# Optimization experiments

Hardware: AMD Instinct MI355X
Metric: run time of the kernel (lower is better)

The kernel has to match this reference:

```python
import jax, jax.numpy as jnp
import numpy as np

B, T, Z, S, H = 32, 128, 100, 6, 64
F1, F2 = 512, 128


def setup_inputs() -> dict:
    key = jax.random.key(0)
    ks = jax.random.split(key, 11)
    g = lambda k, shape, sc: (jax.random.normal(k, shape, dtype=jnp.float32) * sc)
    return {
        "x": jax.random.normal(ks[0], (B, T, Z, S), dtype=jnp.float32),
        "W_ih": g(ks[1], (3 * H, S), 0.125),   # GRU input weights [r|z|n]
        "W_hh": g(ks[2], (3 * H, H), 0.125),   # GRU hidden weights [r|z|n]
        "b_ih": g(ks[3], (3 * H,), 0.125),
        "b_hh": g(ks[4], (3 * H,), 0.125),
        "w1": g(ks[5], (F1, H), 0.1),
        "b1": g(ks[6], (F1,), 0.1),
        "w2": g(ks[7], (F2, F1), 0.04),
        "b2": g(ks[8], (F2,), 0.04),
        "w3": g(ks[9], (1, F2), 0.09),
        "b3": g(ks[10], (1,), 0.09),
    }


def reference(x, W_ih, W_hh, b_ih, b_hh, w1, b1, w2, b2, w3, b3):
    b, t, z, s = x.shape
    h_dim = W_hh.shape[1]
    # Fuse the per-zone python loop into the batch dim, zone-major so the
    # final reshape matches torch.stack(a).view(-1, t, nzones).
    xm = jnp.transpose(x, (2, 0, 1, 3)).reshape(z * b, t, s)  # (ZB, T, S)
    # Precompute input projections for all timesteps (one big GEMM).
    gi_all = jnp.einsum('nts,gs->ntg', xm, W_ih) + b_ih        # (ZB, T, 3H)

    def step(h, gi):
        gh = h @ W_hh.T + b_hh
        r = jax.nn.sigmoid(gi[:, :h_dim] + gh[:, :h_dim])
        zg = jax.nn.sigmoid(gi[:, h_dim:2 * h_dim] + gh[:, h_dim:2 * h_dim])
        n = jnp.tanh(gi[:, 2 * h_dim:] + r * gh[:, 2 * h_dim:])
        h_new = (1.0 - zg) * n + zg * h
        return h_new, h_new

    h0 = jnp.zeros((z * b, h_dim), x.dtype)
    _, sx = jax.lax.scan(step, h0, jnp.swapaxes(gi_all, 0, 1))  # (T, ZB, H)
    sx = jnp.swapaxes(sx, 0, 1)                                  # (ZB, T, H)

    a1 = jax.nn.relu(sx @ w1.T + b1)
    a2 = jax.nn.relu(a1 @ w2.T + b2)
    a3 = a2 @ w3.T + b3                                          # (ZB, T, 1)
    return a3.reshape(-1, t, z)                                  # (B, T, Z)
```

## Files before the change

### kernel.cpp

```cpp
#include <hip/hip_runtime.h>
#include <stdint.h>

#define Tdim 128
#define Zdim 100
#define Sdim 6
#define Hdim 64
#define ZB   3200
#define F1   512
#define F2   128
#define Mrows (ZB * Tdim)

typedef _Float16 f16x8 __attribute__((ext_vector_type(8)));
typedef _Float16 f16x4 __attribute__((ext_vector_type(4)));
typedef float f32x4 __attribute__((ext_vector_type(4)));
typedef uint32_t u32x4 __attribute__((ext_vector_type(4)));

__device__ __forceinline__ float sigmoidf_fast(float x) {
  return 1.f / (1.f + __expf(-x));
}
__device__ __forceinline__ float tanhf_fast(float x) {
  return 1.f - 2.f / (__expf(2.f * x) + 1.f);
}

__global__ __launch_bounds__(256) void prep_kernel(
    const float* __restrict__ W_ih, const float* __restrict__ W_hh,
    const float* __restrict__ w1, const float* __restrict__ w2,
    _Float16* __restrict__ Wf, _Float16* __restrict__ w1p,
    _Float16* __restrict__ w2p) {
  int i = blockIdx.x * 256 + threadIdx.x;
  if (i < 192 * 96) {
    int g = i / 96, k = i - g * 96;
    float v = (k < 64) ? W_hh[g * 64 + k] : ((k < 70) ? W_ih[g * 6 + (k - 64)] : 0.f);
    Wf[i] = (_Float16)v;
  }
  int j = i - 192 * 96;
  if (j >= 0 && j < 32768) {
    int kt = j >> 11, ntl = (j >> 10) & 1, kf = (j >> 9) & 1;
    int lane = (j >> 3) & 63, e = j & 7;
    int q = lane >> 4, c = lane & 15;
    int row = kt * 32 + ntl * 16 + c;
    int h = kf * 32 + q * 8 + e;
    w1p[j] = (_Float16)w1[row * 64 + h];
  }
  int l = j - 32768;
  if (l >= 0 && l < 65536) {
    int kt = l >> 12, nt = (l >> 9) & 7;
    int lane = (l >> 3) & 63, e = l & 7;
    int q = lane >> 4, c = lane & 15;
    int row = nt * 16 + c;
    int k = kt * 32 + q * 8 + e;
    w2p[l] = (_Float16)w2[row * 512 + k];
  }
}

__global__ __launch_bounds__(256, 1) void gru_kernel(
    const float* __restrict__ x, const _Float16* __restrict__ Wf,
    const float* __restrict__ b_ih, const float* __restrict__ b_hh,
    _Float16* __restrict__ sx) {
  __shared__ __align__(16) _Float16 hist[32][16][72];
  __shared__ __align__(16) _Float16 xs[Tdim][16][8];
  const int tid = threadIdx.x;
  const int lane = tid & 63;
  const int w = tid >> 6;
  const int c = lane & 15;
  const int q = lane >> 4;

  for (int i = 0; i < 8; i++) {
    int idx = i * 256 + tid;
    int t = idx >> 4, row = idx & 15;
    int nr = blockIdx.x * 16 + row;
    const float* p = x + (size_t)(nr & 31) * (Tdim * Zdim * Sdim)
                       + (size_t)t * (Zdim * Sdim) + (size_t)(nr >> 5) * Sdim;
    f16x8 v;
    v[0] = (_Float16)p[0]; v[1] = (_Float16)p[1]; v[2] = (_Float16)p[2];
    v[3] = (_Float16)p[3]; v[4] = (_Float16)p[4]; v[5] = (_Float16)p[5];
    v[6] = (_Float16)0.f;  v[7] = (_Float16)0.f;
    *(f16x8*)&xs[t][row][0] = v;
  }

  const int gr0 = w * 16;
  const int gz0 = 64 + w * 16;
  const int gn0 = 128 + w * 16;

  f16x8 Ar[3], Az[3], Anh[2], Ani;
#pragma unroll
  for (int kf = 0; kf < 3; kf++) {
    Ar[kf] = *(const f16x8*)(Wf + (size_t)(gr0 + c) * 96 + kf * 32 + q * 8);
    Az[kf] = *(const f16x8*)(Wf + (size_t)(gz0 + c) * 96 + kf * 32 + q * 8);
  }
  Anh[0] = *(const f16x8*)(Wf + (size_t)(gn0 + c) * 96 + q * 8);
  Anh[1] = *(const f16x8*)(Wf + (size_t)(gn0 + c) * 96 + 32 + q * 8);
  Ani    = *(const f16x8*)(Wf + (size_t)(gn0 + c) * 96 + 64 + q * 8);

  f32x4 Cr, Cz, Cnh, Cni;
  {
    f32x4 bir = *(const f32x4*)(b_ih + gr0 + q * 4);
    f32x4 bhr = *(const f32x4*)(b_hh + gr0 + q * 4);
    f32x4 biz = *(const f32x4*)(b_ih + gz0 + q * 4);
    f32x4 bhz = *(const f32x4*)(b_hh + gz0 + q * 4);
#pragma unroll
    for (int r = 0; r < 4; r++) { Cr[r] = bir[r] + bhr[r]; Cz[r] = biz[r] + bhz[r]; }
    Cnh = *(const f32x4*)(b_hh + gn0 + q * 4);
    Cni = *(const f32x4*)(b_ih + gn0 + q * 4);
  }

  __syncthreads();

  f16x8 Bh0 = {0, 0, 0, 0, 0, 0, 0, 0};
  f16x8 Bh1 = {0, 0, 0, 0, 0, 0, 0, 0};
  f32x4 hprev = {0.f, 0.f, 0.f, 0.f};
  const f32x4 zero4 = {0.f, 0.f, 0.f, 0.f};

  f32x4 Dr_s, Dz_s, Dni_s;
  {
    f16x8 xv8 = *(const f16x8*)&xs[0][c][0];
    f16x8 Bx;
#pragma unroll
    for (int j = 0; j < 8; j++) Bx[j] = (q == 0) ? xv8[j] : (_Float16)0.f;
    Dni_s = __builtin_amdgcn_mfma_f32_16x16x32_f16(Ani, Bx, Cni, 0, 0, 0);
    Dr_s  = __builtin_amdgcn_mfma_f32_16x16x32_f16(Ar[2], Bx, Cr, 0, 0, 0);
    Dz_s  = __builtin_amdgcn_mfma_f32_16x16x32_f16(Az[2], Bx, Cz, 0, 0, 0);
  }

#pragma unroll 1
  for (int tch = 0; tch < 4; tch++) {
#pragma unroll 1
    for (int tc = 0; tc < 32; tc++) {
      const int t = tch * 32 + tc;
      f32x4 Dnh0 = __builtin_amdgcn_mfma_f32_16x16x32_f16(Anh[0], Bh0, Cnh, 0, 0, 0);
      f32x4 Dr0  = __builtin_amdgcn_mfma_f32_16x16x32_f16(Ar[0], Bh0, Dr_s, 0, 0, 0);
      f32x4 Dz0  = __builtin_amdgcn_mfma_f32_16x16x32_f16(Az[0], Bh0, Dz_s, 0, 0, 0);
      f32x4 Dnh1 = __builtin_amdgcn_mfma_f32_16x16x32_f16(Anh[1], Bh1, zero4, 0, 0, 0);
      f32x4 Dr1  = __builtin_amdgcn_mfma_f32_16x16x32_f16(Ar[1], Bh1, zero4, 0, 0, 0);
      f32x4 Dz1  = __builtin_amdgcn_mfma_f32_16x16x32_f16(Az[1], Bh1, zero4, 0, 0, 0);

      f16x4 pk;
#pragma unroll
      for (int r = 0; r < 4; r++) {
        float rr = sigmoidf_fast(Dr0[r] + Dr1[r]);
        float zg = sigmoidf_fast(Dz0[r] + Dz1[r]);
        float nn = tanhf_fast(Dni_s[r] + rr * (Dnh0[r] + Dnh1[r]));
        float hnew = nn + zg * (hprev[r] - nn);
        hprev[r] = hnew;
        pk[r] = (_Float16)hnew;
      }
      *(f16x4*)&hist[tc][c][w * 16 + q * 4] = pk;

      if (t + 1 < Tdim) {
        f16x8 xv8 = *(const f16x8*)&xs[t + 1][c][0];
        f16x8 Bx;
#pragma unroll
        for (int j = 0; j < 8; j++) Bx[j] = (q == 0) ? xv8[j] : (_Float16)0.f;
        Dni_s = __builtin_amdgcn_mfma_f32_16x16x32_f16(Ani, Bx, Cni, 0, 0, 0);
        Dr_s  = __builtin_amdgcn_mfma_f32_16x16x32_f16(Ar[2], Bx, Cr, 0, 0, 0);
        Dz_s  = __builtin_amdgcn_mfma_f32_16x16x32_f16(Az[2], Bx, Cz, 0, 0, 0);
      }
      __syncthreads();
      Bh0 = *(const f16x8*)&hist[tc][c][q * 8];
      Bh1 = *(const f16x8*)&hist[tc][c][32 + q * 8];
    }
    {
      const int t0 = tch * 32;
#pragma unroll
      for (int rr2 = 0; rr2 < 4; rr2++) {
        const int row = w * 4 + rr2;
        const int nrow = blockIdx.x * 16 + row;
        _Float16* dst = sx + (size_t)nrow * Tdim * Hdim + (size_t)t0 * Hdim;
#pragma unroll
        for (int it = 0; it < 4; it++) {
          int idx = it * 64 + lane;
          int tcc = idx >> 3, hd8 = idx & 7;
          f16x8 vv = *(const f16x8*)&hist[tcc][row][hd8 * 8];
          *(f16x8*)(dst + tcc * 64 + hd8 * 8) = vv;
        }
      }
      __syncthreads();
    }
  }
}

__global__ __launch_bounds__(256, 2) void mlp_kernel(
    const _Float16* __restrict__ sx, const _Float16* __restrict__ w1p,
    const _Float16* __restrict__ w2p, const float* __restrict__ b1,
    const float* __restrict__ b2, const float* __restrict__ w3,
    const float* __restrict__ b3, float* __restrict__ out) {
  __shared__ __align__(16) _Float16 rep[4][4][512];
  const int tid = threadIdx.x;
  const int lane = tid & 63;
  const int wave = tid >> 6;
  const int c = lane & 15;
  const int q = lane >> 4;
  const size_t m0 = ((size_t)blockIdx.x * 4 + wave) * 64;

  f16x8 Bs[4][2];
#pragma unroll
  for (int g = 0; g < 4; g++)
#pragma unroll
    for (int kk = 0; kk < 2; kk++)
      Bs[g][kk] = *(const f16x8*)(sx + (m0 + g * 16 + c) * Hdim + kk * 32 + q * 8);

  f32x4 acc2[4][8];
#pragma unroll
  for (int g = 0; g < 4; g++)
#pragma unroll
    for (int nt = 0; nt < 8; nt++) acc2[g][nt] = (f32x4){0.f, 0.f, 0.f, 0.f};

#pragma unroll 2
  for (int kt = 0; kt < 16; kt++) {
    const _Float16* w1g = w1p + (size_t)kt * 2048 + lane * 8;
    const _Float16* w2g = w2p + (size_t)kt * 4096 + lane * 8;
    f16x8 A10 = *(const f16x8*)(w1g);
    f16x8 A11 = *(const f16x8*)(w1g + 512);
    f16x8 A12 = *(const f16x8*)(w1g + 1024);
    f16x8 A13 = *(const f16x8*)(w1g + 1536);

#pragma unroll
    for (int ntl = 0; ntl < 2; ntl++) {
      const int f1b = kt * 32 + ntl * 16;
      f16x8 A0 = ntl ? A12 : A10;
      f16x8 A1 = ntl ? A13 : A11;
      f32x4 bb = *(const f32x4*)(b1 + f1b + q * 4);
      const int roff = ((2 * ntl + (q >> 1)) * 16 + c) * 8 + (q & 1) * 4;
#pragma unroll
      for (int g = 0; g < 4; g++) {
        f32x4 cc = __builtin_amdgcn_mfma_f32_16x16x32_f16(A0, Bs[g][0], bb, 0, 0, 0);
        cc = __builtin_amdgcn_mfma_f32_16x16x32_f16(A1, Bs[g][1], cc, 0, 0, 0);
        f16x4 pk;
#pragma unroll
        for (int r = 0; r < 4; r++)
          pk[r] = (_Float16)(cc[r] > 0.f ? cc[r] : 0.f);
        *(f16x4*)&rep[wave][g][roff] = pk;
      }
    }
    f16x8 W2[8];
#pragma unroll
    for (int nt = 0; nt < 8; nt++)
      W2[nt] = *(const f16x8*)(w2g + nt * 512);
    f16x8 Ba[4];
#pragma unroll
    for (int g = 0; g < 4; g++)
      Ba[g] = *(const f16x8*)&rep[wave][g][lane * 8];
#pragma unroll
    for (int nt = 0; nt < 8; nt++) {
#pragma unroll
      for (int g = 0; g < 4; g++)
        acc2[g][nt] = __builtin_amdgcn_mfma_f32_16x16x32_f16(W2[nt], Ba[g], acc2[g][nt], 0, 0, 0);
    }
  }

  float part[4] = {0.f, 0.f, 0.f, 0.f};
#pragma unroll
  for (int nt = 0; nt < 8; nt++) {
    f32x4 bb = *(const f32x4*)(b2 + nt * 16 + q * 4);
    f32x4 ww = *(const f32x4*)(w3 + nt * 16 + q * 4);
#pragma unroll
    for (int g = 0; g < 4; g++) {
#pragma unroll
      for (int r = 0; r < 4; r++) {
        float v = acc2[g][nt][r] + bb[r];
        v = v > 0.f ? v : 0.f;
        part[g] = fmaf(v, ww[r], part[g]);
      }
    }
  }
#pragma unroll
  for (int g = 0; g < 4; g++) {
    part[g] += __shfl_xor(part[g], 16, 64);
    part[g] += __shfl_xor(part[g], 32, 64);
  }
  float pv = (q == 0) ? part[0] : (q == 1) ? part[1] : (q == 2) ? part[2] : part[3];
  out[m0 + q * 16 + c] = pv + b3[0];
}

extern "C" void kernel_launch(void* const* d_in, const int* in_sizes, int n_in,
                              void* d_out, int out_size, void* d_ws, size_t ws_size,
                              hipStream_t stream) {
  const float* x    = (const float*)d_in[0];
  const float* W_ih = (const float*)d_in[1];
  const float* W_hh = (const float*)d_in[2];
  const float* b_ih = (const float*)d_in[3];
  const float* b_hh = (const float*)d_in[4];
  const float* w1   = (const float*)d_in[5];
  const float* b1   = (const float*)d_in[6];
  const float* w2   = (const float*)d_in[7];
  const float* b2   = (const float*)d_in[8];
  const float* w3   = (const float*)d_in[9];
  const float* b3   = (const float*)d_in[10];
  float* out = (float*)d_out;

  char* ws = (char*)d_ws;
  _Float16* sxf = (_Float16*)ws;
  _Float16* Wf  = (_Float16*)(ws + 52428800);
  _Float16* w1p = (_Float16*)(ws + 52428800 + 36864);
  _Float16* w2p = (_Float16*)(ws + 52428800 + 36864 + 65536);

  hipLaunchKernelGGL(prep_kernel, dim3(456), dim3(256), 0, stream,
                     W_ih, W_hh, w1, w2, Wf, w1p, w2p);
  hipLaunchKernelGGL(gru_kernel, dim3(ZB / 16), dim3(256), 0, stream,
                     x, Wf, b_ih, b_hh, sxf);
  hipLaunchKernelGGL(mlp_kernel, dim3(Mrows / 256), dim3(256), 0, stream,
                     sxf, w1p, w2p, b1, b2, w3, b3, out);
}
```

Baseline: 257.9 us.

## Fuse GRU recurrence with MLP head, overlapping MLP on previous chunk

Merges the GRU and MLP kernels into one kernel. The MLP for the previous 16-timestep chunk runs interleaved with the serial GRU steps of the current chunk, using a double-buffered shared-memory history. This removes the 50 MB fp16 hidden-state round trip through global memory and uses idle MFMA/VALU slots in the latency-bound recurrence. The cost is that only 200 blocks do all the MLP work with one block per CU, and register pressure rises, which risks spills and a longer serial critical path.

```diff
diff --git a/kernel.cpp b/kernel.cpp
--- a/kernel.cpp
+++ b/kernel.cpp
@@ -8,12 +8,10 @@
 #define ZB   3200
 #define F1   512
 #define F2   128
-#define Mrows (ZB * Tdim)
 
 typedef _Float16 f16x8 __attribute__((ext_vector_type(8)));
 typedef _Float16 f16x4 __attribute__((ext_vector_type(4)));
 typedef float f32x4 __attribute__((ext_vector_type(4)));
-typedef uint32_t u32x4 __attribute__((ext_vector_type(4)));
 
 __device__ __forceinline__ float sigmoidf_fast(float x) {
   return 1.f / (1.f + __expf(-x));
@@ -53,12 +51,16 @@
   }
 }
 
-__global__ __launch_bounds__(256, 1) void gru_kernel(
+__global__ __launch_bounds__(256, 1) void fused_kernel(
     const float* __restrict__ x, const _Float16* __restrict__ Wf,
     const float* __restrict__ b_ih, const float* __restrict__ b_hh,
-    _Float16* __restrict__ sx) {
-  __shared__ __align__(16) _Float16 hist[32][16][72];
+    const _Float16* __restrict__ w1p, const _Float16* __restrict__ w2p,
+    const float* __restrict__ b1, const float* __restrict__ b2,
+    const float* __restrict__ w3, const float* __restrict__ b3,
+    float* __restrict__ out) {
+  __shared__ __align__(16) _Float16 hist[2][16][16][72];
   __shared__ __align__(16) _Float16 xs[Tdim][16][8];
+  __shared__ __align__(16) _Float16 rep[4][2][512];
   const int tid = threadIdx.x;
   const int lane = tid & 63;
   const int w = tid >> 6;
@@ -104,6 +106,9 @@
     Cni = *(const f32x4*)(b_ih + gn0 + q * 4);
   }
 
+  const int n = blockIdx.x * 16 + c;
+  const float b3v = b3[0];
+
   __syncthreads();
 
   f16x8 Bh0 = {0, 0, 0, 0, 0, 0, 0, 0};
@@ -123,153 +128,195 @@
   }
 
 #pragma unroll 1
-  for (int tch = 0; tch < 4; tch++) {
-#pragma unroll 1
-    for (int tc = 0; tc < 32; tc++) {
-      const int t = tch * 32 + tc;
-      f32x4 Dnh0 = __builtin_amdgcn_mfma_f32_16x16x32_f16(Anh[0], Bh0, Cnh, 0, 0, 0);
-      f32x4 Dr0  = __builtin_amdgcn_mfma_f32_16x16x32_f16(Ar[0], Bh0, Dr_s, 0, 0, 0);
-      f32x4 Dz0  = __builtin_amdgcn_mfma_f32_16x16x32_f16(Az[0], Bh0, Dz_s, 0, 0, 0);
-      f32x4 Dnh1 = __builtin_amdgcn_mfma_f32_16x16x32_f16(Anh[1], Bh1, zero4, 0, 0, 0);
-      f32x4 Dr1  = __builtin_amdgcn_mfma_f32_16x16x32_f16(Ar[1], Bh1, zero4, 0, 0, 0);
-      f32x4 Dz1  = __builtin_amdgcn_mfma_f32_16x16x32_f16(Az[1], Bh1, zero4, 0, 0, 0);
-
-      f16x4 pk;
-#pragma unroll
-      for (int r = 0; r < 4; r++) {
-        float rr = sigmoidf_fast(Dr0[r] + Dr1[r]);
-        float zg = sigmoidf_fast(Dz0[r] + Dz1[r]);
-        float nn = tanhf_fast(Dni_s[r] + rr * (Dnh0[r] + Dnh1[r]));
-        float hnew = nn + zg * (hprev[r] - nn);
-        hprev[r] = hnew;
-        pk[r] = (_Float16)hnew;
-      }
-      *(f16x4*)&hist[tc][c][w * 16 + q * 4] = pk;
-
-      if (t + 1 < Tdim) {
-        f16x8 xv8 = *(const f16x8*)&xs[t + 1][c][0];
-        f16x8 Bx;
-#pragma unroll
-        for (int j = 0; j < 8; j++) Bx[j] = (q == 0) ? xv8[j] : (_Float16)0.f;
-        Dni_s = __builtin_amdgcn_mfma_f32_16x16x32_f16(Ani, Bx, Cni, 0, 0, 0);
-        Dr_s  = __builtin_amdgcn_mfma_f32_16x16x32_f16(Ar[2], Bx, Cr, 0, 0, 0);
-        Dz_s  = __builtin_amdgcn_mfma_f32_16x16x32_f16(Az[2], Bx, Cz, 0, 0, 0);
-      }
-      __syncthreads();
-      Bh0 = *(const f16x8*)&hist[tc][c][q * 8];
-      Bh1 = *(const f16x8*)&hist[tc][c][32 + q * 8];
+  for (int tch = 0; tch < 8; tch++) {
+    const int buf = tch & 1;
+#pragma unroll 1
+    for (int p = 0; p < 2; p++) {
+      const bool mlp = (tch > 0);
+      f16x8 Bs[2][2];
+      f32x4 acc2[2][8];
+      if (mlp) {
+#pragma unroll
+        for (int gi = 0; gi < 2; gi++) {
+          const int tcg = w * 4 + p * 2 + gi;
+          Bs[gi][0] = *(const f16x8*)&hist[buf ^ 1][tcg][c][q * 8];
+          Bs[gi][1] = *(const f16x8*)&hist[buf ^ 1][tcg][c][32 + q * 8];
+#pragma unroll
+          for (int nt = 0; nt < 8; nt++) acc2[gi][nt] = zero4;
+        }
+      }
+#pragma unroll 1
+      for (int sp = 0; sp < 8; sp++) {
+        const int tc = p * 8 + sp;
+        const int t = tch * 16 + tc;
+        f16x8 W1v[2][4], W2v[2][8];
+        f32x4 bb1[2][2];
+        if (mlp) {
+#pragma unroll
+          for (int kk = 0; kk < 2; kk++) {
+            const int kt = sp * 2 + kk;
+            const _Float16* w1g = w1p + (size_t)kt * 2048 + lane * 8;
+            const _Float16* w2g = w2p + (size_t)kt * 4096 + lane * 8;
+#pragma unroll
+            for (int f = 0; f < 4; f++) W1v[kk][f] = *(const f16x8*)(w1g + f * 512);
+#pragma unroll
+            for (int nt = 0; nt < 8; nt++) W2v[kk][nt] = *(const f16x8*)(w2g + nt * 512);
+            bb1[kk][0] = *(const f32x4*)(b1 + kt * 32 + q * 4);
+            bb1[kk][1] = *(const f32x4*)(b1 + kt * 32 + 16 + q * 4);
+          }
+        }
+        f32x4 Dnh0 = __builtin_amdgcn_mfma_f32_16x16x32_f16(Anh[0], Bh0, Cnh, 0, 0, 0);
+        f32x4 Dr0  = __builtin_amdgcn_mfma_f32_16x16x32_f16(Ar[0], Bh0, Dr_s, 0, 0, 0);
+        f32x4 Dz0  = __builtin_amdgcn_mfma_f32_16x16x32_f16(Az[0], Bh0, Dz_s, 0, 0, 0);
+        f32x4 Dnh1 = __builtin_amdgcn_mfma_f32_16x16x32_f16(Anh[1], Bh1, zero4, 0, 0, 0);
+        f32x4 Dr1  = __builtin_amdgcn_mfma_f32_16x16x32_f16(Ar[1], Bh1, zero4, 0, 0, 0);
+        f32x4 Dz1  = __builtin_amdgcn_mfma_f32_16x16x32_f16(Az[1], Bh1, zero4, 0, 0, 0);
+
+        f16x4 pk;
+#pragma unroll
+        for (int r = 0; r < 4; r++) {
+          float rr = sigmoidf_fast(Dr0[r] + Dr1[r]);
+          float zg = sigmoidf_fast(Dz0[r] + Dz1[r]);
+          float nn = tanhf_fast(Dni_s[r] + rr * (Dnh0[r] + Dnh1[r]));
+          float hnew = nn + zg * (hprev[r] - nn);
+          hprev[r] = hnew;
+          pk[r] = (_Float16)hnew;
+        }
+        *(f16x4*)&hist[buf][tc][c][w * 16 + q * 4] = pk;
+
+        if (t + 1 < Tdim) {
+          f16x8 xv8 = *(const f16x8*)&xs[t + 1][c][0];
+          f16x8 Bx;
+#pragma unroll
+          for (int j = 0; j < 8; j++) Bx[j] = (q == 0) ? xv8[j] : (_Float16)0.f;
+          Dni_s = __builtin_amdgcn_mfma_f32_16x16x32_f16(Ani, Bx, Cni, 0, 0, 0);
+          Dr_s  = __builtin_amdgcn_mfma_f32_16x16x32_f16(Ar[2], Bx, Cr, 0, 0, 0);
+          Dz_s  = __builtin_amdgcn_mfma_f32_16x16x32_f16(Az[2], Bx, Cz, 0, 0, 0);
+        }
+
+        if (mlp) {
+#pragma unroll
+          for (int kk = 0; kk < 2; kk++) {
+#pragma unroll
+            for (int ntl = 0; ntl < 2; ntl++) {
+              const int roff = ((2 * ntl + (q >> 1)) * 16 + c) * 8 + (q & 1) * 4;
+#pragma unroll
+              for (int gi = 0; gi < 2; gi++) {
+                f32x4 cc = __builtin_amdgcn_mfma_f32_16x16x32_f16(W1v[kk][ntl * 2], Bs[gi][0], bb1[kk][ntl], 0, 0, 0);
+                cc = __builtin_amdgcn_mfma_f32_16x16x32_f16(W1v[kk][ntl * 2 + 1], Bs[gi][1], cc, 0, 0, 0);
+                f16x4 pk2;
+#pragma unroll
+                for (int r = 0; r < 4; r++)
+                  pk2[r] = (_Float16)(cc[r] > 0.f ? cc[r] : 0.f);
+                *(f16x4*)&rep[w][gi][roff] = pk2;
+              }
+            }
+            f16x8 Ba[2];
+#pragma unroll
+            for (int gi = 0; gi < 2; gi++)
+              Ba[gi] = *(const f16x8*)&rep[w][gi][lane * 8];
+#pragma unroll
+            for (int nt = 0; nt < 8; nt++)
+#pragma unroll
+              for (int gi = 0; gi < 2; gi++)
+                acc2[gi][nt] = __builtin_amdgcn_mfma_f32_16x16x32_f16(W2v[kk][nt], Ba[gi], acc2[gi][nt], 0, 0, 0);
+          }
+        }
+        __syncthreads();
+        Bh0 = *(const f16x8*)&hist[buf][tc][c][q * 8];
+        Bh1 = *(const f16x8*)&hist[buf][tc][c][32 + q * 8];
+      }
+      if (mlp) {
+#pragma unroll
+        for (int gi = 0; gi < 2; gi++) {
+          float part = 0.f;
+#pragma unroll
+          for (int nt = 0; nt < 8; nt++) {
+            f32x4 bb = *(const f32x4*)(b2 + nt * 16 + q * 4);
+            f32x4 ww = *(const f32x4*)(w3 + nt * 16 + q * 4);
+#pragma unroll
+            for (int r = 0; r < 4; r++) {
+              float v = acc2[gi][nt][r] + bb[r];
+              v = v > 0.f ? v : 0.f;
+              part = fmaf(v, ww[r], part);
+            }
+          }
+          part += __shfl_xor(part, 16, 64);
+          part += __shfl_xor(part, 32, 64);
+          if (q == 0)
+            out[(size_t)n * Tdim + (tch - 1) * 16 + w * 4 + p * 2 + gi] = part + b3v;
+        }
+      }
     }
-    {
-      const int t0 = tch * 32;
-#pragma unroll
-      for (int rr2 = 0; rr2 < 4; rr2++) {
-        const int row = w * 4 + rr2;
-        const int nrow = blockIdx.x * 16 + row;
-        _Float16* dst = sx + (size_t)nrow * Tdim * Hdim + (size_t)t0 * Hdim;
-#pragma unroll
-        for (int it = 0; it < 4; it++) {
-          int idx = it * 64 + lane;
-          int tcc = idx >> 3, hd8 = idx & 7;
-          f16x8 vv = *(const f16x8*)&hist[tcc][row][hd8 * 8];
-          *(f16x8*)(dst + tcc * 64 + hd8 * 8) = vv;
-        }
-      }
-      __syncthreads();
+  }
+
+#pragma unroll 1
+  for (int p = 0; p < 2; p++) {
+    f16x8 Bs[2][2];
+    f32x4 acc2[2][8];
+#pragma unroll
+    for (int gi = 0; gi < 2; gi++) {
+      const int tcg = w * 4 + p * 2 + gi;
+      Bs[gi][0] = *(const f16x8*)&hist[1][tcg][c][q * 8];
+      Bs[gi][1] = *(const f16x8*)&hist[1][tcg][c][32 + q * 8];
+#pragma unroll
+      for (int nt = 0; nt < 8; nt++) acc2[gi][nt] = (f32x4){0.f, 0.f, 0.f, 0.f};
     }
-  }
-}
-
-__global__ __launch_bounds__(256, 2) void mlp_kernel(
-    const _Float16* __restrict__ sx, const _Float16* __restrict__ w1p,
-    const _Float16* __restrict__ w2p, const float* __restrict__ b1,
-    const float* __restrict__ b2, const float* __restrict__ w3,
-    const float* __restrict__ b3, float* __restrict__ out) {
-  __shared__ __align__(16) _Float16 rep[4][4][512];
-  const int tid = threadIdx.x;
-  const int lane = tid & 63;
-  const int wave = tid >> 6;
-  const int c = lane & 15;
-  const int q = lane >> 4;
-  const size_t m0 = ((size_t)blockIdx.x * 4 + wave) * 64;
-
-  f16x8 Bs[4][2];
-#pragma unroll
-  for (int g = 0; g < 4; g++)
-#pragma unroll
-    for (int kk = 0; kk < 2; kk++)
-      Bs[g][kk] = *(const f16x8*)(sx + (m0 + g * 16 + c) * Hdim + kk * 32 + q * 8);
-
-  f32x4 acc2[4][8];
-#pragma unroll
-  for (int g = 0; g < 4; g++)
-#pragma unroll
-    for (int nt = 0; nt < 8; nt++) acc2[g][nt] = (f32x4){0.f, 0.f, 0.f, 0.f};
-
-#pragma unroll 2
-  for (int kt = 0; kt < 16; kt++) {
-    const _Float16* w1g = w1p + (size_t)kt * 2048 + lane * 8;
-    const _Float16* w2g = w2p + (size_t)kt * 4096 + lane * 8;
-    f16x8 A10 = *(const f16x8*)(w1g);
-    f16x8 A11 = *(const f16x8*)(w1g + 512);
-    f16x8 A12 = *(const f16x8*)(w1g + 1024);
-    f16x8 A13 = *(const f16x8*)(w1g + 1536);
-
-#pragma unroll
-    for (int ntl = 0; ntl < 2; ntl++) {
-      const int f1b = kt * 32 + ntl * 16;
-      f16x8 A0 = ntl ? A12 : A10;
-      f16x8 A1 = ntl ? A13 : A11;
-      f32x4 bb = *(const f32x4*)(b1 + f1b + q * 4);
-      const int roff = ((2 * ntl + (q >> 1)) * 16 + c) * 8 + (q & 1) * 4;
-#pragma unroll
-      for (int g = 0; g < 4; g++) {
-        f32x4 cc = __builtin_amdgcn_mfma_f32_16x16x32_f16(A0, Bs[g][0], bb, 0, 0, 0);
-        cc = __builtin_amdgcn_mfma_f32_16x16x32_f16(A1, Bs[g][1], cc, 0, 0, 0);
-        f16x4 pk;
-#pragma unroll
-        for (int r = 0; r < 4; r++)
-          pk[r] = (_Float16)(cc[r] > 0.f ? cc[r] : 0.f);
-        *(f16x4*)&rep[wave][g][roff] = pk;
-      }
+#pragma unroll 1
+    for (int kt = 0; kt < 16; kt++) {
+      const _Float16* w1g = w1p + (size_t)kt * 2048 + lane * 8;
+      const _Float16* w2g = w2p + (size_t)kt * 4096 + lane * 8;
+      f16x8 W1v[4], W2v[8];
+#pragma unroll
+      for (int f = 0; f < 4; f++) W1v[f] = *(const f16x8*)(w1g + f * 512);
+#pragma unroll
+      for (int nt = 0; nt < 8; nt++) W2v[nt] = *(const f16x8*)(w2g + nt * 512);
+      f32x4 bb1a = *(const f32x4*)(b1 + kt * 32 + q * 4);
+      f32x4 bb1b = *(const f32x4*)(b1 + kt * 32 + 16 + q * 4);
+#pragma unroll
+      for (int ntl = 0; ntl < 2; ntl++) {
+        const int roff = ((2 * ntl + (q >> 1)) * 16 + c) * 8 + (q & 1) * 4;
+#pragma unroll
+        for (int gi = 0; gi < 2; gi++) {
+          f32x4 cc = __builtin_amdgcn_mfma_f32_16x16x32_f16(W1v[ntl * 2], Bs[gi][0], ntl ? bb1b : bb1a, 0, 0, 0);
+          cc = __builtin_amdgcn_mfma_f32_16x16x32_f16(W1v[ntl * 2 + 1], Bs[gi][1], cc, 0, 0, 0);
+          f16x4 pk2;
+#pragma unroll
+          for (int r = 0; r < 4; r++)
+            pk2[r] = (_Float16)(cc[r] > 0.f ? cc[r] : 0.f);
+          *(f16x4*)&rep[w][gi][roff] = pk2;
+        }
+      }
+      f16x8 Ba[2];
+#pragma unroll
+      for (int gi = 0; gi < 2; gi++)
+        Ba[gi] = *(const f16x8*)&rep[w][gi][lane * 8];
+#pragma unroll
+      for (int nt = 0; nt < 8; nt++)
+#pragma unroll
+        for (int gi = 0; gi < 2; gi++)
+          acc2[gi][nt] = __builtin_amdgcn_mfma_f32_16x16x32_f16(W2v[nt], Ba[gi], acc2[gi][nt], 0, 0, 0);
     }
-    f16x8 W2[8];
-#pragma unroll
-    for (int nt = 0; nt < 8; nt++)
-      W2[nt] = *(const f16x8*)(w2g + nt * 512);
-    f16x8 Ba[4];
-#pragma unroll
-    for (int g = 0; g < 4; g++)
-      Ba[g] = *(const f16x8*)&rep[wave][g][lane * 8];
-#pragma unroll
-    for (int nt = 0; nt < 8; nt++) {
-#pragma unroll
-      for (int g = 0; g < 4; g++)
-        acc2[g][nt] = __builtin_amdgcn_mfma_f32_16x16x32_f16(W2[nt], Ba[g], acc2[g][nt], 0, 0, 0);
+#pragma unroll
+    for (int gi = 0; gi < 2; gi++) {
+      float part = 0.f;
+#pragma unroll
+      for (int nt = 0; nt < 8; nt++) {
+        f32x4 bb = *(const f32x4*)(b2 + nt * 16 + q * 4);
+        f32x4 ww = *(const f32x4*)(w3 + nt * 16 + q * 4);
+#pragma unroll
+        for (int r = 0; r < 4; r++) {
+          float v = acc2[gi][nt][r] + bb[r];
+          v = v > 0.f ? v : 0.f;
+          part = fmaf(v, ww[r], part);
+        }
+      }
+      part += __shfl_xor(part, 16, 64);
+      part += __shfl_xor(part, 32, 64);
+      if (q == 0)
+        out[(size_t)n * Tdim + 7 * 16 + w * 4 + p * 2 + gi] = part + b3v;
     }
   }
-
-  float part[4] = {0.f, 0.f, 0.f, 0.f};
-#pragma unroll
-  for (int nt = 0; nt < 8; nt++) {
-    f32x4 bb = *(const f32x4*)(b2 + nt * 16 + q * 4);
-    f32x4 ww = *(const f32x4*)(w3 + nt * 16 + q * 4);
-#pragma unroll
-    for (int g = 0; g < 4; g++) {
-#pragma unroll
-      for (int r = 0; r < 4; r++) {
-        float v = acc2[g][nt][r] + bb[r];
-        v = v > 0.f ? v : 0.f;
-        part[g] = fmaf(v, ww[r], part[g]);
-      }
-    }
-  }
-#pragma unroll
-  for (int g = 0; g < 4; g++) {
-    part[g] += __shfl_xor(part[g], 16, 64);
-    part[g] += __shfl_xor(part[g], 32, 64);
-  }
-  float pv = (q == 0) ? part[0] : (q == 1) ? part[1] : (q == 2) ? part[2] : part[3];
-  out[m0 + q * 16 + c] = pv + b3[0];
 }
 
 extern "C" void kernel_launch(void* const* d_in, const int* in_sizes, int n_in,
@@ -289,15 +336,12 @@
   float* out = (float*)d_out;
 
   char* ws = (char*)d_ws;
-  _Float16* sxf = (_Float16*)ws;
-  _Float16* Wf  = (_Float16*)(ws + 52428800);
-  _Float16* w1p = (_Float16*)(ws + 52428800 + 36864);
-  _Float16* w2p = (_Float16*)(ws + 52428800 + 36864 + 65536);
+  _Float16* Wf  = (_Float16*)ws;
+  _Float16* w1p = (_Float16*)(ws + 36864);
+  _Float16* w2p = (_Float16*)(ws + 36864 + 65536);
 
   hipLaunchKernelGGL(prep_kernel, dim3(456), dim3(256), 0, stream,
                      W_ih, W_hh, w1, w2, Wf, w1p, w2p);
-  hipLaunchKernelGGL(gru_kernel, dim3(ZB / 16), dim3(256), 0, stream,
-                     x, Wf, b_ih, b_hh, sxf);
-  hipLaunchKernelGGL(mlp_kernel, dim3(Mrows / 256), dim3(256), 0, stream,
-                     sxf, w1p, w2p, b1, b2, w3, b3, out);
-}
+  hipLaunchKernelGGL(fused_kernel, dim3(ZB / 16), dim3(256), 0, stream,
+                     x, Wf, b_ih, b_hh, w1p, w2p, b1, b2, w3, b3, out);
+}
```

Result: slower. 389.3 us (+51.0%).
